# Performance work log

Hardware: AMD Instinct MI355X
Metric: run time of the kernel (lower is better)

The kernel has to match this reference:

```python
import jax, jax.numpy as jnp
import numpy as np

EMBED = 1024
HEADS = 16
HEAD_DIM = EMBED // HEADS


def setup_inputs() -> dict:
    key = jax.random.key(0)
    ks = jax.random.split(key, 6)
    B, S, E = 2, 2048, EMBED
    x = jax.random.normal(ks[0], (B, S, E), dtype=jnp.float32)
    # torch nn.Linear stores weight as [out, in]; scale ~ 1/sqrt(E) like default init
    sc = 1.0 / np.sqrt(E)
    Wq = jax.random.normal(ks[1], (E, E), dtype=jnp.float32) * sc
    Wk = jax.random.normal(ks[2], (E, E), dtype=jnp.float32) * sc
    Wv = jax.random.normal(ks[3], (E, E), dtype=jnp.float32) * sc
    Wo = jax.random.normal(ks[4], (E, E), dtype=jnp.float32) * sc
    bo = jnp.zeros((E,), dtype=jnp.float32)
    # causal mask, broadcastable [1,1,S,S]; mask==0 positions get -inf
    mask = jnp.tril(jnp.ones((S, S), dtype=jnp.int32))[None, None]
    return {"x": x, "mask": mask, "Wq": Wq, "Wk": Wk, "Wv": Wv, "Wo": Wo, "bo": bo}


def reference(x, mask, Wq, Wk, Wv, Wo, bo):
    B, S, E = x.shape
    # Linear(x) = x @ W.T (torch convention, no bias)
    Q = (x @ Wq.T).reshape(B, S, HEADS, HEAD_DIM).transpose(0, 2, 1, 3)  # [B,H,S,D]
    K = (x @ Wk.T).reshape(B, S, HEADS, HEAD_DIM).transpose(0, 2, 1, 3)
    V = (x @ Wv.T).reshape(B, S, HEADS, HEAD_DIM).transpose(0, 2, 1, 3)
    scale = 1.0 / jnp.sqrt(jnp.float32(HEAD_DIM))
    scores = jnp.einsum("bhqd,bhkd->bhqk", Q, K) * scale  # [B,H,S,S]
    scores = jnp.where(mask == 0, -jnp.inf, scores)
    attn = jax.nn.softmax(scores, axis=-1)
    out = jnp.einsum("bhqk,bhkd->bhqd", attn, V)  # [B,H,S,D]
    out = out.transpose(0, 2, 1, 3).reshape(B, S, E)
    return out @ Wo.T + bo
```

## Files before the change

kernel.cpp:

```cpp
#include <hip/hip_runtime.h>
#include <hip/hip_bf16.h>

typedef unsigned short u16;
typedef unsigned int u32;

#define B_ 2
#define S_ 2048
#define E_ 1024
#define H_ 16
#define D_ 64

typedef __bf16 bf16_8 __attribute__((ext_vector_type(8)));
typedef __bf16 bf16_4 __attribute__((ext_vector_type(4)));
typedef float f32_4 __attribute__((ext_vector_type(4)));

typedef const __attribute__((address_space(1))) void* gptr_t;
typedef __attribute__((address_space(3))) void* sptr_t;

__device__ __forceinline__ void gload_lds16(const void* g, void* l) {
  __builtin_amdgcn_global_load_lds((gptr_t)g, (sptr_t)l, 16, 0, 0);
}

__device__ __forceinline__ u16 f2bf(float f) {
  union { float f; u32 u; } v; v.f = f;
  u32 u = v.u;
  u32 r = (u + 0x7FFFu + ((u >> 16) & 1u)) >> 16;
  return (u16)r;
}

__global__ __launch_bounds__(256) void cvt_all(
    const float* __restrict__ x,
    const float* __restrict__ wq, const float* __restrict__ wk,
    const float* __restrict__ wv, const float* __restrict__ wo,
    u16* __restrict__ dst)
{
  const int XB = (B_ * S_ * E_) / 1024;
  const int WB = (E_ * E_) / 1024;
  int blk = blockIdx.x;
  const float* src;
  size_t dbase;
  if (blk < XB)           { src = x;  dbase = 0;                         }
  else if (blk < XB+WB)   { src = wq; dbase = (size_t)B_*S_*E_;          blk -= XB; }
  else if (blk < XB+2*WB) { src = wk; dbase = (size_t)B_*S_*E_ + E_*E_;  blk -= XB+WB; }
  else if (blk < XB+3*WB) { src = wv; dbase = (size_t)B_*S_*E_ + 2*(size_t)E_*E_; blk -= XB+2*WB; }
  else                    { src = wo; dbase = (size_t)B_*S_*E_ + 3*(size_t)E_*E_; blk -= XB+3*WB; }
  size_t i = ((size_t)blk * 256 + threadIdx.x) * 4;
  float4 v = *(const float4*)(src + i);
  ushort4 o;
  o.x = f2bf(v.x); o.y = f2bf(v.y); o.z = f2bf(v.z); o.w = f2bf(v.w);
  *(ushort4*)(dst + dbase + i) = o;
}

#define MFMA16 __builtin_amdgcn_mfma_f32_16x16x32_bf16
#define BARX() asm volatile("s_barrier" ::: "memory")

__global__ __launch_bounds__(512, 2) void qkv_gemm(
    const u16* __restrict__ x,
    const u16* __restrict__ wq, const u16* __restrict__ wk, const u16* __restrict__ wv,
    u16* __restrict__ q_ws, u16* __restrict__ k_ws, u16* __restrict__ v_ws)
{
  const int K = E_;
  __shared__ __attribute__((aligned(16))) u16 SM[65536];

  int tid = threadIdx.x;
  int wave = tid >> 6, lane = tid & 63;
  int quad = lane >> 4, fcol = lane & 15;
  int wr = wave >> 2, wc = wave & 3;
  int swzb = fcol & 7;

  int my = ((blockIdx.x & 7) * 24) + (blockIdx.x >> 3);
  int rb = my / 12, cb = my % 12;
  int row0 = rb << 8;
  int which = cb >> 2;
  const u16* W = (which == 0) ? wq : ((which == 1) ? wk : wv);
  int col0 = (cb & 3) << 8;

  auto stg = [&](const u16* src, int srow0, int buf, int bofs, int h, int k0) {
#pragma unroll
    for (int i = 0; i < 2; i++) {
      int c = (i << 9) + tid;
      int r = c >> 3;
      int kcd = (c & 7) ^ (r & 7);
      gload_lds16(src + (size_t)(srow0 + h * 128 + r) * K + k0 + kcd * 8,
                  SM + buf * 32768 + bofs + ((h << 10) + c) * 8);
    }
  };

  f32_4 acc[8][4];
#pragma unroll
  for (int i = 0; i < 8; i++)
#pragma unroll
    for (int j = 0; j < 4; j++) acc[i][j] = f32_4{0.f, 0.f, 0.f, 0.f};

  stg(W, col0, 0, 16384, 0, 0);
  stg(x, row0, 0, 0,     0, 0);
  stg(W, col0, 0, 16384, 1, 0);
  stg(x, row0, 0, 0,     1, 0);
  stg(W, col0, 1, 16384, 0, 64);
  stg(x, row0, 1, 0,     0, 64);
  asm volatile("s_waitcnt vmcnt(4)" ::: "memory");
  BARX();

  int arow = wr * 128 + fcol;
  int brow = wc * 64 + fcol;
  int xo0 = (quad ^ swzb) << 3;
  int xo1 = ((4 + quad) ^ swzb) << 3;

  bf16_8 a[2][4], bl[2][2], bh[2][2];

  for (int kt = 0; kt < 16; ++kt) {
    int bj = kt & 1;
    const u16* Ab = SM + bj * 32768;
    const u16* Bb = Ab + 16384;

#pragma unroll
    for (int mt = 0; mt < 4; mt++) {
      a[0][mt] = *(const bf16_8*)(Ab + (arow + mt * 16) * 64 + xo0);
      a[1][mt] = *(const bf16_8*)(Ab + (arow + mt * 16) * 64 + xo1);
    }
#pragma unroll
    for (int nt = 0; nt < 2; nt++) {
      bl[0][nt] = *(const bf16_8*)(Bb + (brow + nt * 16) * 64 + xo0);
      bl[1][nt] = *(const bf16_8*)(Bb + (brow + nt * 16) * 64 + xo1);
    }
    if (kt + 1 < 16) stg(W, col0, bj ^ 1, 16384, 1, (kt + 1) * 64);
    BARX();
    __builtin_amdgcn_s_setprio(1);
#pragma unroll
    for (int ks = 0; ks < 2; ks++)
#pragma unroll
      for (int mt = 0; mt < 4; mt++)
#pragma unroll
        for (int nt = 0; nt < 2; nt++)
          acc[mt][nt] = MFMA16(a[ks][mt], bl[ks][nt], acc[mt][nt], 0, 0, 0);
    __builtin_amdgcn_s_setprio(0);
    BARX();

#pragma unroll
    for (int nt = 0; nt < 2; nt++) {
      bh[0][nt] = *(const bf16_8*)(Bb + (brow + (nt + 2) * 16) * 64 + xo0);
      bh[1][nt] = *(const bf16_8*)(Bb + (brow + (nt + 2) * 16) * 64 + xo1);
    }
    if (kt + 1 < 16) stg(x, row0, bj ^ 1, 0, 1, (kt + 1) * 64);
    BARX();
    __builtin_amdgcn_s_setprio(1);
#pragma unroll
    for (int ks = 0; ks < 2; ks++)
#pragma unroll
      for (int mt = 0; mt < 4; mt++)
#pragma unroll
        for (int nt = 0; nt < 2; nt++)
          acc[mt][2 + nt] = MFMA16(a[ks][mt], bh[ks][nt], acc[mt][2 + nt], 0, 0, 0);
    __builtin_amdgcn_s_setprio(0);
    BARX();

#pragma unroll
    for (int mt = 0; mt < 4; mt++) {
      a[0][mt] = *(const bf16_8*)(Ab + (arow + (mt + 4) * 16) * 64 + xo0);
      a[1][mt] = *(const bf16_8*)(Ab + (arow + (mt + 4) * 16) * 64 + xo1);
    }
    if (kt + 2 < 16) stg(W, col0, bj, 16384, 0, (kt + 2) * 64);
    BARX();
    __builtin_amdgcn_s_setprio(1);
#pragma unroll
    for (int ks = 0; ks < 2; ks++)
#pragma unroll
      for (int mt = 0; mt < 4; mt++)
#pragma unroll
        for (int nt = 0; nt < 2; nt++)
          acc[4 + mt][2 + nt] = MFMA16(a[ks][mt], bh[ks][nt], acc[4 + mt][2 + nt], 0, 0, 0);
    __builtin_amdgcn_s_setprio(0);
    BARX();

    if (kt + 2 < 16) stg(x, row0, bj, 0, 0, (kt + 2) * 64);
    if (kt + 2 < 16) {
      asm volatile("s_waitcnt vmcnt(4)" ::: "memory");
    } else if (kt + 1 < 16) {
      asm volatile("s_waitcnt vmcnt(0)" ::: "memory");
    }
    BARX();
    __builtin_amdgcn_s_setprio(1);
#pragma unroll
    for (int ks = 0; ks < 2; ks++)
#pragma unroll
      for (int mt = 0; mt < 4; mt++)
#pragma unroll
        for (int nt = 0; nt < 2; nt++)
          acc[4 + mt][nt] = MFMA16(a[ks][mt], bl[ks][nt], acc[4 + mt][nt], 0, 0, 0);
    __builtin_amdgcn_s_setprio(0);
    BARX();
  }

  u16* scr = SM + wave * 8192;
  int h = ((cb & 3) << 2) + wc;
  int grow0 = row0 + wr * 128;
  int bb = grow0 >> 11, srow0 = grow0 & (S_ - 1);

  if (which != 2) {
#pragma unroll
    for (int m = 0; m < 8; m++)
#pragma unroll
      for (int n = 0; n < 4; n++)
#pragma unroll
        for (int r = 0; r < 4; r++) {
          int s = m * 16 + quad * 4 + r;
          int d = n * 16 + fcol;
          scr[s * 64 + (((d >> 3) ^ (s & 7)) << 3) + (d & 7)] = f2bf(acc[m][n][r]);
        }
    __syncthreads();
    u16* dst = (which == 0) ? q_ws : k_ws;
    u16* gp = dst + (((size_t)bb * H_ + h) * S_ + srow0) * D_;
    int lrow = lane >> 3, cc = lane & 7;
#pragma unroll
    for (int i = 0; i < 16; i++) {
      int sl = i * 8 + lrow;
      *(bf16_8*)(gp + (size_t)sl * D_ + cc * 8) =
          *(const bf16_8*)(scr + sl * 64 + ((cc ^ (sl & 7)) << 3));
    }
  } else {
#pragma unroll
    for (int m = 0; m < 8; m++)
#pragma unroll
      for (int n = 0; n < 4; n++)
#pragma unroll
        for (int r = 0; r < 4; r++) {
          int s = m * 16 + quad * 4 + r;
          int d = n * 16 + fcol;
          scr[d * 128 + (((s >> 3) ^ (d & 15)) << 3) + (s & 7)] = f2bf(acc[m][n][r]);
        }
    __syncthreads();
    size_t base2 = (((size_t)bb * H_ + h) * D_) * S_ + srow0;
    int lrow = lane >> 4, cc = lane & 15;
#pragma unroll
    for (int i = 0; i < 16; i++) {
      int dl = i * 4 + lrow;
      *(bf16_8*)(v_ws + base2 + (size_t)dl * S_ + cc * 8) =
          *(const bf16_8*)(scr + dl * 128 + ((cc ^ (dl & 15)) << 3));
    }
  }
}

#define AST 72
#define PST 68
__global__ __launch_bounds__(256, 4) void attn_kernel(
    const u16* __restrict__ Qg_, const u16* __restrict__ Kg_,
    const u16* __restrict__ Vg_, u16* __restrict__ Og_)
{
  __shared__ __attribute__((aligned(16))) u16 Ks[64 * AST];
  __shared__ __attribute__((aligned(16))) u16 Vs[64 * AST];
  __shared__ __attribute__((aligned(16))) u16 Ps[4 * 16 * PST];

  int tid = threadIdx.x, wave = tid >> 6, lane = tid & 63;
  int quad = lane >> 4, fcol = lane & 15;
  int blk = blockIdx.x;
  int bh = blk & 31;
  int k = 31 - (blk >> 5);
  int b = bh >> 4, h = bh & (H_ - 1);

  const u16* Qg = Qg_ + (size_t)bh * S_ * D_;
  const u16* Kg = Kg_ + (size_t)bh * S_ * D_;
  const u16* Vg = Vg_ + (size_t)bh * D_ * S_;

  int qb = k * 64 + wave * 16;

  bf16_8 aq[2];
#pragma unroll
  for (int ks2 = 0; ks2 < 2; ks2++)
    aq[ks2] = *(const bf16_8*)(Qg + (size_t)(qb + fcol) * D_ + ks2 * 32 + quad * 8);

  const __bf16 one = (__bf16)1.0f;
  const bf16_8 vone = {one, one, one, one, one, one, one, one};

  f32_4 accO[4];
  f32_4 accL = f32_4{0.f, 0.f, 0.f, 0.f};
#pragma unroll
  for (int nt = 0; nt < 4; nt++) accO[nt] = f32_4{0.f, 0.f, 0.f, 0.f};

  u16* Pw = Ps + wave * 16 * PST;

  for (int j = 0; j <= k; j++) {
#pragma unroll
    for (int i = 0; i < 2; i++) {
      int c = i * 256 + tid;
      int r = c >> 3, cc = (c & 7) * 8;
      *(bf16_8*)(Ks + r * AST + cc) =
          *(const bf16_8*)(Kg + (size_t)(j * 64 + r) * D_ + cc);
      *(bf16_8*)(Vs + r * AST + cc) =
          *(const bf16_8*)(Vg + (size_t)r * S_ + j * 64 + cc);
    }
    __syncthreads();

    f32_4 sc[4];
#pragma unroll
    for (int nt = 0; nt < 4; nt++) sc[nt] = f32_4{0.f, 0.f, 0.f, 0.f};
#pragma unroll
    for (int ks2 = 0; ks2 < 2; ks2++) {
#pragma unroll
      for (int nt = 0; nt < 4; nt++) {
        bf16_8 bk = *(const bf16_8*)(Ks + (nt * 16 + fcol) * AST + ks2 * 32 + quad * 8);
        sc[nt] = __builtin_amdgcn_mfma_f32_16x16x32_bf16(aq[ks2], bk, sc[nt], 0, 0, 0);
      }
    }

    bool partial = (j == k);
    int qrow0 = qb + quad * 4;
    float p[4][4];
#pragma unroll
    for (int nt = 0; nt < 4; nt++) {
      int kv = j * 64 + nt * 16 + fcol;
#pragma unroll
      for (int r = 0; r < 4; r++) {
        float e = __expf(fmaf(sc[nt][r], 0.125f, -12.0f));
        p[nt][r] = (!partial || kv <= qrow0 + r) ? e : 0.f;
      }
    }

#pragma unroll
    for (int nt = 0; nt < 4; nt++)
#pragma unroll
      for (int r = 0; r < 4; r++)
        Pw[(quad * 4 + r) * PST + nt * 16 + fcol] = f2bf(p[nt][r]);

#pragma unroll
    for (int ks2 = 0; ks2 < 2; ks2++) {
      const u16* ab = Pw + fcol * PST + ks2 * 32 + quad * 8;
      bf16_4 lo = *(const bf16_4*)(ab);
      bf16_4 hi = *(const bf16_4*)(ab + 4);
      bf16_8 ap = __builtin_shufflevector(lo, hi, 0, 1, 2, 3, 4, 5, 6, 7);
      accL = __builtin_amdgcn_mfma_f32_16x16x32_bf16(ap, vone, accL, 0, 0, 0);
#pragma unroll
      for (int nt = 0; nt < 4; nt++) {
        bf16_8 bv = *(const bf16_8*)(Vs + (nt * 16 + fcol) * AST + ks2 * 32 + quad * 8);
        accO[nt] = __builtin_amdgcn_mfma_f32_16x16x32_bf16(ap, bv, accO[nt], 0, 0, 0);
      }
    }
    __syncthreads();
  }

#pragma unroll
  for (int r = 0; r < 4; r++) {
    float inv = 1.0f / accL[r];
    int qrow = qb + quad * 4 + r;
#pragma unroll
    for (int nt = 0; nt < 4; nt++) {
      int d = nt * 16 + fcol;
      Og_[((size_t)b * S_ + qrow) * E_ + h * D_ + d] = f2bf(accO[nt][r] * inv);
    }
  }
}

__global__ __launch_bounds__(256) void out_gemm(
    const u16* __restrict__ A, const u16* __restrict__ W,
    const float* __restrict__ bias, float* __restrict__ out)
{
  const int K = E_;
  __shared__ __attribute__((aligned(16))) u16 As[128 * 64];
  __shared__ __attribute__((aligned(16))) u16 Bs[64 * 64];

  int tid = threadIdx.x;
  int wave = tid >> 6, lane = tid & 63;
  int quad = lane >> 4, fcol = lane & 15;
  int row0 = blockIdx.x * 128;
  int col0 = blockIdx.y * 64;
  int swzb = fcol & 7;

  f32_4 acc[2][4];
#pragma unroll
  for (int i = 0; i < 2; i++)
#pragma unroll
    for (int j = 0; j < 4; j++) acc[i][j] = f32_4{0.f, 0.f, 0.f, 0.f};

  for (int k0 = 0; k0 < K; k0 += 64) {
#pragma unroll
    for (int i = 0; i < 4; i++) {
      int c = i * 256 + tid;
      int r = c >> 3;
      int kcd = (c & 7) ^ (r & 7);
      gload_lds16(A + (size_t)(row0 + r) * K + k0 + kcd * 8, As + (size_t)c * 8);
    }
#pragma unroll
    for (int i = 0; i < 2; i++) {
      int c = i * 256 + tid;
      int r = c >> 3;
      int kcd = (c & 7) ^ (r & 7);
      gload_lds16(W + (size_t)(col0 + r) * K + k0 + kcd * 8, Bs + (size_t)c * 8);
    }
    __syncthreads();
#pragma unroll
    for (int ks2 = 0; ks2 < 2; ks2++) {
      bf16_8 a[2], b[4];
#pragma unroll
      for (int mt = 0; mt < 2; mt++) {
        int rm = wave * 32 + mt * 16 + fcol;
        a[mt] = *(const bf16_8*)(As + rm * 64 + (((ks2 * 4 + quad) ^ swzb) << 3));
      }
#pragma unroll
      for (int nt = 0; nt < 4; nt++) {
        int rn = nt * 16 + fcol;
        b[nt] = *(const bf16_8*)(Bs + rn * 64 + (((ks2 * 4 + quad) ^ swzb) << 3));
      }
#pragma unroll
      for (int mt = 0; mt < 2; mt++)
#pragma unroll
        for (int nt = 0; nt < 4; nt++)
          acc[mt][nt] = __builtin_amdgcn_mfma_f32_16x16x32_bf16(a[mt], b[nt], acc[mt][nt], 0, 0, 0);
    }
    __syncthreads();
  }

#pragma unroll
  for (int mt = 0; mt < 2; mt++)
#pragma unroll
    for (int nt = 0; nt < 4; nt++) {
      int gcol = col0 + nt * 16 + fcol;
      float bv = bias[gcol];
#pragma unroll
      for (int r = 0; r < 4; r++) {
        int grow = row0 + wave * 32 + mt * 16 + quad * 4 + r;
        out[(size_t)grow * E_ + gcol] = acc[mt][nt][r] + bv;
      }
    }
}

extern "C" void kernel_launch(void* const* d_in, const int* in_sizes, int n_in,
                              void* d_out, int out_size, void* d_ws, size_t ws_size,
                              hipStream_t stream) {
  const float* x  = (const float*)d_in[0];
  const float* wq = (const float*)d_in[2];
  const float* wk = (const float*)d_in[3];
  const float* wv = (const float*)d_in[4];
  const float* wo = (const float*)d_in[5];
  const float* bo = (const float*)d_in[6];
  float* out = (float*)d_out;

  const size_t sz  = (size_t)B_ * S_ * E_;
  const size_t wsz = (size_t)E_ * E_;
  if (ws_size < (5 * sz + 4 * wsz) * sizeof(u16)) return;

  u16* x_bf  = (u16*)d_ws;
  u16* wq_bf = x_bf + sz;
  u16* wk_bf = wq_bf + wsz;
  u16* wv_bf = wk_bf + wsz;
  u16* wo_bf = wv_bf + wsz;
  u16* q_ws  = wo_bf + wsz;
  u16* k_ws  = q_ws + sz;
  u16* v_ws  = k_ws + sz;
  u16* o_ws  = v_ws + sz;

  cvt_all<<<(int)((sz + 4 * wsz) / 1024), 256, 0, stream>>>(x, wq, wk, wv, wo, x_bf);
  qkv_gemm<<<dim3(192), 512, 0, stream>>>(x_bf, wq_bf, wk_bf, wv_bf, q_ws, k_ws, v_ws);
  attn_kernel<<<dim3(1024), 256, 0, stream>>>(q_ws, k_ws, v_ws, o_ws);
  out_gemm<<<dim3(32, 16), 256, 0, stream>>>(o_ws, wo_bf, bo, out);
}
```

Measured before the change: 184.2 us.

## Double-buffer K/V with async LDS loads, swizzle LDS, rebalance causal tiles

The attention kernel now prefetches the next K/V tile into a second LDS buffer with direct global-to-LDS loads while it computes on the current tile. The padded LDS layouts are replaced by XOR-swizzled layouts for K, V and P. Blocks are mapped to query tiles in an interleaved order to balance causal work across the grid. It also raises wave priority around the MFMA sections and applies the causal mask only on the diagonal tile. The main risk is synchronisation: the loop barrier has no explicit vmcnt wait for the async prefetch, so correctness relies on the compiler inserting one.

```diff
diff --git a/kernel.cpp b/kernel.cpp
--- a/kernel.cpp
+++ b/kernel.cpp
@@ -240,21 +240,20 @@
   }
 }
 
-#define AST 72
-#define PST 68
 __global__ __launch_bounds__(256, 4) void attn_kernel(
     const u16* __restrict__ Qg_, const u16* __restrict__ Kg_,
     const u16* __restrict__ Vg_, u16* __restrict__ Og_)
 {
-  __shared__ __attribute__((aligned(16))) u16 Ks[64 * AST];
-  __shared__ __attribute__((aligned(16))) u16 Vs[64 * AST];
-  __shared__ __attribute__((aligned(16))) u16 Ps[4 * 16 * PST];
+  __shared__ __attribute__((aligned(16))) u16 KV[16384];
+  __shared__ __attribute__((aligned(16))) u16 Ps[4096];
 
   int tid = threadIdx.x, wave = tid >> 6, lane = tid & 63;
   int quad = lane >> 4, fcol = lane & 15;
   int blk = blockIdx.x;
   int bh = blk & 31;
-  int k = 31 - (blk >> 5);
+  int g = blk >> 5;
+  int r8 = g & 7, q4 = g >> 3;
+  int k = (q4 == 0) ? (31 - r8) : ((q4 == 1) ? (16 + r8) : ((q4 == 2) ? (15 - r8) : r8));
   int b = bh >> 4, h = bh & (H_ - 1);
 
   const u16* Qg = Qg_ + (size_t)bh * S_ * D_;
@@ -262,12 +261,29 @@
   const u16* Vg = Vg_ + (size_t)bh * D_ * S_;
 
   int qb = k * 64 + wave * 16;
+  int sw = fcol & 7;
 
   bf16_8 aq[2];
 #pragma unroll
   for (int ks2 = 0; ks2 < 2; ks2++)
     aq[ks2] = *(const bf16_8*)(Qg + (size_t)(qb + fcol) * D_ + ks2 * 32 + quad * 8);
 
+  auto stage = [&](int j, int buf) {
+    u16* Kb = KV + buf * 8192;
+#pragma unroll
+    for (int i = 0; i < 2; i++) {
+      int c = (i << 8) + tid;
+      int r = c >> 3;
+      int kcd = (c & 7) ^ (r & 7);
+      gload_lds16(Kg + (size_t)(j * 64 + r) * D_ + kcd * 8, Kb + c * 8);
+      gload_lds16(Vg + (size_t)r * S_ + j * 64 + kcd * 8, Kb + 4096 + c * 8);
+    }
+  };
+
+  stage(0, 0);
+  asm volatile("s_waitcnt vmcnt(0)" ::: "memory");
+  __syncthreads();
+
   const __bf16 one = (__bf16)1.0f;
   const bf16_8 vone = {one, one, one, one, one, one, one, one};
 
@@ -276,65 +292,68 @@
 #pragma unroll
   for (int nt = 0; nt < 4; nt++) accO[nt] = f32_4{0.f, 0.f, 0.f, 0.f};
 
-  u16* Pw = Ps + wave * 16 * PST;
+  u16* Pw = Ps + wave * 1024;
 
   for (int j = 0; j <= k; j++) {
-#pragma unroll
-    for (int i = 0; i < 2; i++) {
-      int c = i * 256 + tid;
-      int r = c >> 3, cc = (c & 7) * 8;
-      *(bf16_8*)(Ks + r * AST + cc) =
-          *(const bf16_8*)(Kg + (size_t)(j * 64 + r) * D_ + cc);
-      *(bf16_8*)(Vs + r * AST + cc) =
-          *(const bf16_8*)(Vg + (size_t)r * S_ + j * 64 + cc);
-    }
-    __syncthreads();
+    const u16* Kb = KV + (j & 1) * 8192;
+    const u16* Vb = Kb + 4096;
+    if (j < k) stage(j + 1, (j & 1) ^ 1);
 
     f32_4 sc[4];
 #pragma unroll
     for (int nt = 0; nt < 4; nt++) sc[nt] = f32_4{0.f, 0.f, 0.f, 0.f};
+    __builtin_amdgcn_s_setprio(1);
 #pragma unroll
     for (int ks2 = 0; ks2 < 2; ks2++) {
 #pragma unroll
       for (int nt = 0; nt < 4; nt++) {
-        bf16_8 bk = *(const bf16_8*)(Ks + (nt * 16 + fcol) * AST + ks2 * 32 + quad * 8);
-        sc[nt] = __builtin_amdgcn_mfma_f32_16x16x32_bf16(aq[ks2], bk, sc[nt], 0, 0, 0);
-      }
-    }
-
-    bool partial = (j == k);
-    int qrow0 = qb + quad * 4;
+        bf16_8 bk = *(const bf16_8*)(Kb + (nt * 16 + fcol) * 64 + (((ks2 * 4 + quad) ^ sw) << 3));
+        sc[nt] = MFMA16(aq[ks2], bk, sc[nt], 0, 0, 0);
+      }
+    }
+    __builtin_amdgcn_s_setprio(0);
+
     float p[4][4];
 #pragma unroll
+    for (int nt = 0; nt < 4; nt++)
+#pragma unroll
+      for (int r = 0; r < 4; r++)
+        p[nt][r] = __expf(fmaf(sc[nt][r], 0.125f, -12.0f));
+    if (j == k) {
+      int qrow0 = qb + quad * 4;
+#pragma unroll
+      for (int nt = 0; nt < 4; nt++) {
+        int kv = j * 64 + nt * 16 + fcol;
+#pragma unroll
+        for (int r = 0; r < 4; r++)
+          if (kv > qrow0 + r) p[nt][r] = 0.f;
+      }
+    }
+
+#pragma unroll
     for (int nt = 0; nt < 4; nt++) {
-      int kv = j * 64 + nt * 16 + fcol;
+      int ch = nt * 2 + (fcol >> 3);
 #pragma unroll
       for (int r = 0; r < 4; r++) {
-        float e = __expf(fmaf(sc[nt][r], 0.125f, -12.0f));
-        p[nt][r] = (!partial || kv <= qrow0 + r) ? e : 0.f;
-      }
-    }
-
-#pragma unroll
-    for (int nt = 0; nt < 4; nt++)
-#pragma unroll
-      for (int r = 0; r < 4; r++)
-        Pw[(quad * 4 + r) * PST + nt * 16 + fcol] = f2bf(p[nt][r]);
-
+        int row = quad * 4 + r;
+        Pw[row * 64 + ((ch ^ (row & 7)) << 3) + (fcol & 7)] = f2bf(p[nt][r]);
+      }
+    }
+
+    __builtin_amdgcn_s_setprio(1);
 #pragma unroll
     for (int ks2 = 0; ks2 < 2; ks2++) {
-      const u16* ab = Pw + fcol * PST + ks2 * 32 + quad * 8;
-      bf16_4 lo = *(const bf16_4*)(ab);
-      bf16_4 hi = *(const bf16_4*)(ab + 4);
-      bf16_8 ap = __builtin_shufflevector(lo, hi, 0, 1, 2, 3, 4, 5, 6, 7);
-      accL = __builtin_amdgcn_mfma_f32_16x16x32_bf16(ap, vone, accL, 0, 0, 0);
+      bf16_8 ap = *(const bf16_8*)(Pw + fcol * 64 + (((ks2 * 4 + quad) ^ sw) << 3));
+      accL = MFMA16(ap, vone, accL, 0, 0, 0);
 #pragma unroll
       for (int nt = 0; nt < 4; nt++) {
-        bf16_8 bv = *(const bf16_8*)(Vs + (nt * 16 + fcol) * AST + ks2 * 32 + quad * 8);
-        accO[nt] = __builtin_amdgcn_mfma_f32_16x16x32_bf16(ap, bv, accO[nt], 0, 0, 0);
-      }
-    }
-    __syncthreads();
+        bf16_8 bv = *(const bf16_8*)(Vb + (nt * 16 + fcol) * 64 + (((ks2 * 4 + quad) ^ sw) << 3));
+        accO[nt] = MFMA16(ap, bv, accO[nt], 0, 0, 0);
+      }
+    }
+    __builtin_amdgcn_s_setprio(0);
+
+    if (j < k) __syncthreads();
   }
 
 #pragma unroll
```

Result: no change. 186.4 us (+1.2%).
